# Kernel tuning notes

Measured on AMD Instinct MI355X. Metric: run time of the kernel, lower is better.

The kernel has to match this reference:

```python
import jax, jax.numpy as jnp
import numpy as np


def setup_inputs() -> dict:
    key = jax.random.key(0)
    k1, k2, k3, k4 = jax.random.split(key, 4)
    B, S, D, F = 16, 4096, 1024, 1024
    x = jax.random.normal(k1, (B, S, D), dtype=jnp.float32)
    # Keras 'normal' initializer ~ N(0, 0.05); scale similarly for realism
    W_key = jax.random.normal(k2, (D, F), dtype=jnp.float32) * 0.05
    W_query = jax.random.normal(k3, (D, F), dtype=jnp.float32) * 0.05
    W_value = jax.random.normal(k4, (D, F), dtype=jnp.float32) * 0.05
    return {"x": x, "W_key": W_key, "W_query": W_query, "W_value": W_value}


def reference(x, W_key, W_query, W_value):
    # x: [B,S,D]; W_*: [D,F]
    keys = jnp.tanh(jnp.einsum("bsd,df->bsf", x, W_key))
    query = jnp.tanh(jnp.einsum("bsd,df->bsf", x, W_query))
    value = jnp.tanh(jnp.einsum("bsd,df->bsf", x, W_value))
    # diag(Q K^T) == per-token dot product, computed directly in O(S*F)
    attn_scores = jnp.einsum("bsf,bsf->bs", query, keys)  # [B,S]
    attn_softmax = jax.nn.softmax(attn_scores, axis=-1)[..., None]  # [B,S,1]
    # value^T @ softmax -> [B,F,1]
    weighted_input = jnp.einsum("bsf,bso->bfo", value, attn_softmax)
    return weighted_input, attn_softmax
```

## Files before the change

kernel.cpp:

```cpp
#include <hip/hip_runtime.h>
#include <hip/hip_bf16.h>
#include <math.h>
#include <stdint.h>

typedef _Float16 f16;
typedef _Float16 half8 __attribute__((ext_vector_type(8)));
typedef float f32x4 __attribute__((ext_vector_type(4)));

#define B_ 16
#define S_ 4096
#define D_ 1024
#define F_ 1024
#define TOK (B_*S_)
#define TB3 128
#define FB3 64
#define NFB3 16
#define NT3 32
#define NSV 4
#define CSV (S_/NSV)

__device__ __forceinline__ void gload_lds16(const void* g, void* l) {
    __builtin_amdgcn_global_load_lds(
        (__attribute__((address_space(1))) const unsigned int*)(unsigned long long)(uintptr_t)g,
        (__attribute__((address_space(3))) unsigned int*)(unsigned int)(uintptr_t)l,
        16, 0, 0);
}

__device__ __forceinline__ void fma4(float4& a, float s, const float4& wv) {
    a.x += s * wv.x; a.y += s * wv.y; a.z += s * wv.z; a.w += s * wv.w;
}
__device__ __forceinline__ void wtanh4(float4& acc, float pw, const float4& a) {
    acc.x += pw * tanhf(a.x); acc.y += pw * tanhf(a.y);
    acc.z += pw * tanhf(a.z); acc.w += pw * tanhf(a.w);
}

__global__ void cvt_x(const float* __restrict__ x, f16* __restrict__ xh) {
    size_t i = ((size_t)blockIdx.x * 256 + threadIdx.x) * 8;
    float4 a = *(const float4*)(x + i);
    float4 b = *(const float4*)(x + i + 4);
    half8 h = {(f16)a.x,(f16)a.y,(f16)a.z,(f16)a.w,
               (f16)b.x,(f16)b.y,(f16)b.z,(f16)b.w};
    *(half8*)(xh + i) = h;
}

__global__ void cvt_w2(const float* __restrict__ Wk, const float* __restrict__ Wq,
                       f16* __restrict__ wtf) {
    const int gw   = blockIdx.x * 4 + (threadIdx.x >> 6);
    const int lane = threadIdx.x & 63;
    const int nblk = gw & 3, kt = (gw >> 2) & 31, fb = (gw >> 7) & 15, mat = gw >> 11;
    const float* W = mat ? Wq : Wk;
    const int f  = fb * 64 + nblk * 16 + (lane & 15);
    const int d0 = kt * 32 + (lane >> 4) * 8;
    half8 h;
#pragma unroll
    for (int e = 0; e < 8; ++e) h[e] = (f16)W[(size_t)(d0 + e) * F_ + f];
    *(half8*)(wtf + (size_t)gw * 512 + lane * 8) = h;
}

__launch_bounds__(256, 3)
__global__ void score_gemm(const f16* __restrict__ xh, const f16* __restrict__ wtf,
                           float* __restrict__ part) {
    __shared__ __align__(16) f16 Xs[4][TB3 * 32];
    __shared__ float sred[2][TB3];

    const int hid  = blockIdx.x;
    const int orig = (hid & 7) * 1024 + (hid >> 3);
    const int fb   = orig & 15;
    const int tok0 = (orig >> 4) * TB3;

    const int t = threadIdx.x, lane = t & 63, w = t >> 6;
    const int wr = (w >> 1) * 64;
    const int wc = (w & 1) * 32;

    const int rx0 = t >> 2,         qx0 = (t & 3) ^ ((rx0 >> 1) & 3);
    const int rx1 = (t + 256) >> 2, qx1 = (t & 3) ^ ((rx1 >> 1) & 3);
    const f16* srcX0 = xh + (size_t)(tok0 + rx0) * D_ + qx0 * 8;
    const f16* srcX1 = xh + (size_t)(tok0 + rx1) * D_ + qx1 * 8;
    const int wbase = w * 1024;

    int offA[4];
#pragma unroll
    for (int m = 0; m < 4; ++m) {
        int row = wr + m * 16 + (lane & 15);
        int q   = (lane >> 4) ^ ((row >> 1) & 3);
        offA[m] = row * 32 + q * 8;
    }

    const f16* bK = wtf + (((size_t)fb * NT3 * 4) + 2 * (w & 1)) * 512 + lane * 8;
    const f16* bQ = bK + (size_t)NFB3 * NT3 * 4 * 512;

#define STAGE_X(sl, kof) do {                                         \
        gload_lds16(srcX0 + (kof), (char*)Xs[sl] + wbase);            \
        gload_lds16(srcX1 + (kof), (char*)Xs[sl] + 4096 + wbase);     \
    } while (0)

    f32x4 accK[4][2] = {};
    f32x4 accQ[4][2] = {};
    half8 wKf[2][2], wQf[2][2];

    STAGE_X(0, 0);
    STAGE_X(1, 32);
    STAGE_X(2, 64);
#pragma unroll
    for (int n = 0; n < 2; ++n) {
        wKf[0][n] = *(const half8*)(bK + n * 512);
        wQf[0][n] = *(const half8*)(bQ + n * 512);
    }
    asm volatile("s_waitcnt vmcnt(8)" ::: "memory");
    __builtin_amdgcn_s_barrier();

#pragma unroll
    for (int kt = 0; kt < NT3; ++kt) {
        const int cur = kt & 3, par = kt & 1, nx = par ^ 1;
        if (kt < NT3 - 1) {
#pragma unroll
            for (int n = 0; n < 2; ++n) {
                wKf[nx][n] = *(const half8*)(bK + ((size_t)(kt + 1) * 4 + n) * 512);
                wQf[nx][n] = *(const half8*)(bQ + ((size_t)(kt + 1) * 4 + n) * 512);
            }
        }
        if (kt < NT3 - 3) STAGE_X((kt + 3) & 3, (kt + 3) * 32);

        half8 aF[4];
#pragma unroll
        for (int m = 0; m < 4; ++m) aF[m] = *(const half8*)(Xs[cur] + offA[m]);
#pragma unroll
        for (int n = 0; n < 2; ++n)
#pragma unroll
            for (int m = 0; m < 4; ++m) {
                accK[m][n] = __builtin_amdgcn_mfma_f32_16x16x32_f16(aF[m], wKf[par][n], accK[m][n], 0, 0, 0);
                accQ[m][n] = __builtin_amdgcn_mfma_f32_16x16x32_f16(aF[m], wQf[par][n], accQ[m][n], 0, 0, 0);
            }
        if (kt < NT3 - 1) __builtin_amdgcn_s_barrier();
    }
#undef STAGE_X

#pragma unroll
    for (int m = 0; m < 4; ++m) {
        float s[4] = {0.f, 0.f, 0.f, 0.f};
#pragma unroll
        for (int n = 0; n < 2; ++n)
#pragma unroll
            for (int j = 0; j < 4; ++j)
                s[j] += tanhf(accQ[m][n][j]) * tanhf(accK[m][n][j]);
#pragma unroll
        for (int j = 0; j < 4; ++j) {
            s[j] += __shfl_xor(s[j], 1);
            s[j] += __shfl_xor(s[j], 2);
            s[j] += __shfl_xor(s[j], 4);
            s[j] += __shfl_xor(s[j], 8);
        }
        if ((lane & 15) == 0) {
            int g = lane >> 4;
#pragma unroll
            for (int j = 0; j < 4; ++j)
                sred[w & 1][wr + m * 16 + g * 4 + j] = s[j];
        }
    }
    __syncthreads();
    if (t < TB3)
        part[(size_t)fb * TOK + tok0 + t] = sred[0][t] + sred[1][t];
}

__global__ void sum_k(const float* __restrict__ part, float* __restrict__ scores) {
    int i = blockIdx.x * 256 + threadIdx.x;
    float s = 0.f;
#pragma unroll
    for (int fb = 0; fb < NFB3; ++fb) s += part[(size_t)fb * TOK + i];
    scores[i] = s;
}

__global__ void softmax_k(const float* __restrict__ scores, float* __restrict__ out) {
    __shared__ float sc[S_];
    __shared__ float red[256];
    const int b = blockIdx.x, t = threadIdx.x;
    float lmax = -1e30f;
    for (int i = t; i < S_; i += 256) {
        float s = scores[(size_t)b * S_ + i];
        sc[i] = s;
        lmax = fmaxf(lmax, s);
    }
    red[t] = lmax; __syncthreads();
    for (int o = 128; o > 0; o >>= 1) { if (t < o) red[t] = fmaxf(red[t], red[t + o]); __syncthreads(); }
    const float mx = red[0]; __syncthreads();
    float lsum = 0.f;
    for (int i = t; i < S_; i += 256) { float e = expf(sc[i] - mx); sc[i] = e; lsum += e; }
    red[t] = lsum; __syncthreads();
    for (int o = 128; o > 0; o >>= 1) { if (t < o) red[t] += red[t + o]; __syncthreads(); }
    const float inv = 1.0f / red[0];
    for (int i = t; i < S_; i += 256)
        out[(size_t)B_ * F_ + (size_t)b * S_ + i] = sc[i] * inv;
}

__launch_bounds__(256)
__global__ void value_k4(const float* __restrict__ x, const float* __restrict__ Wv,
                         const float* __restrict__ p_in, float* __restrict__ vpart) {
    __shared__ __align__(16) float xs[8][D_];
    __shared__ float ps[CSV];
    __shared__ int   idxs[CSV];
    __shared__ int   wsum[4];
    __shared__ int   rbase_s;
    const int b = blockIdx.x, c = blockIdx.y;
    const int t = threadIdx.x, lane = t & 63, w = t >> 6;
    const int s0 = c * CSV;

    if (t == 0) rbase_s = 0;
    __syncthreads();
#pragma unroll 1
    for (int r = 0; r < 4; ++r) {
        int i = r * 256 + t;
        float p = p_in[(size_t)b * S_ + s0 + i];
        bool flag = p > 1e-7f;
        unsigned long long mask = __ballot(flag);
        if (lane == 0) wsum[w] = __popcll(mask);
        __syncthreads();
        int base = rbase_s;
#pragma unroll
        for (int k = 0; k < 4; ++k) if (k < w) base += wsum[k];
        if (flag) {
            int pos = base + __popcll(mask & ((1ull << lane) - 1ull));
            idxs[pos] = s0 + i;
            ps[pos] = p;
        }
        __syncthreads();
        if (t == 0) rbase_s += wsum[0] + wsum[1] + wsum[2] + wsum[3];
        __syncthreads();
    }
    const int cnt = rbase_s;

    float4 acc = {0.f, 0.f, 0.f, 0.f};
    for (int g = 0; g < cnt; g += 8) {
        __syncthreads();
#pragma unroll
        for (int r = 0; r < 8; ++r) {
            float4 v = {0.f, 0.f, 0.f, 0.f};
            if (g + r < cnt)
                v = ((const float4*)(x + ((size_t)b * S_ + idxs[g + r]) * D_))[t];
            ((float4*)xs[r])[t] = v;
        }
        __syncthreads();
        float4 a[8] = {};
#pragma unroll 2
        for (int dq = 0; dq < D_ / 4; ++dq) {
            const float* wrp = Wv + (size_t)dq * 4 * F_;
            float4 wv0 = ((const float4*)(wrp        ))[t];
            float4 wv1 = ((const float4*)(wrp + F_   ))[t];
            float4 wv2 = ((const float4*)(wrp + 2*F_ ))[t];
            float4 wv3 = ((const float4*)(wrp + 3*F_ ))[t];
#pragma unroll
            for (int r = 0; r < 8; ++r) {
                float4 xr = ((const float4*)xs[r])[dq];
                fma4(a[r], xr.x, wv0); fma4(a[r], xr.y, wv1);
                fma4(a[r], xr.z, wv2); fma4(a[r], xr.w, wv3);
            }
        }
#pragma unroll
        for (int r = 0; r < 8; ++r)
            if (g + r < cnt) wtanh4(acc, ps[g + r], a[r]);
    }
    ((float4*)(vpart + ((size_t)c * B_ + b) * F_))[t] = acc;
}

__global__ void value_red(const float* __restrict__ vpart, float* __restrict__ out) {
    int i = blockIdx.x * 256 + threadIdx.x;
    float s = 0.f;
#pragma unroll
    for (int c = 0; c < NSV; ++c) s += vpart[(size_t)c * B_ * F_ + i];
    out[i] = s;
}

extern "C" void kernel_launch(void* const* d_in, const int* in_sizes, int n_in,
                              void* d_out, int out_size, void* d_ws, size_t ws_size,
                              hipStream_t stream) {
    const float* x  = (const float*)d_in[0];
    const float* Wk = (const float*)d_in[1];
    const float* Wq = (const float*)d_in[2];
    const float* Wv = (const float*)d_in[3];
    float* out = (float*)d_out;
    char* ws = (char*)d_ws;

    f16*   xh     = (f16*)ws;
    f16*   wtf    = (f16*)(ws + (size_t)TOK * D_ * 2);
    float* part   = (float*)(ws + (size_t)TOK * D_ * 2 + 2 * (size_t)D_ * F_ * 2);
    float* scores = part + (size_t)NFB3 * TOK;

    cvt_x<<<TOK * D_ / 8 / 256, 256, 0, stream>>>(x, xh);
    cvt_w2<<<1024, 256, 0, stream>>>(Wk, Wq, wtf);
    score_gemm<<<NFB3 * (TOK / TB3), 256, 0, stream>>>(xh, wtf, part);
    sum_k<<<TOK / 256, 256, 0, stream>>>(part, scores);
    softmax_k<<<B_, 256, 0, stream>>>(scores, out);
    float* vpart = part;
    const float* p_in = out + (size_t)B_ * F_;
    value_k4<<<dim3(B_, NSV), 256, 0, stream>>>(x, Wv, p_in, vpart);
    value_red<<<B_ * F_ / 256, 256, 0, stream>>>(vpart, out);
}
```

Measured before the change: 575.7 us.

## Retile score GEMM to per-wave private X tiles without block barriers

Changes the score GEMM tile from 128 tokens x 64 features to 256 tokens x 32 features. Each wave now stages its own 64-row X slice into a private triple-buffered LDS region, so the per-k-step block barriers and the cross-wave shared reduction go away, and each wave writes its partial scores directly. It also adds s_setprio around the MFMA burst and per-iteration vmcnt waits. The cost is that each X tile is reused by fewer features, so X is reloaded twice as often per feature, and the partial-score buffer plus the sum_k pass over it double in size.

```diff
diff --git a/kernel.cpp b/kernel.cpp
--- a/kernel.cpp
+++ b/kernel.cpp
@@ -12,9 +12,9 @@
 #define D_ 1024
 #define F_ 1024
 #define TOK (B_*S_)
-#define TB3 128
-#define FB3 64
-#define NFB3 16
+#define TB4 256
+#define FB4 32
+#define NFB4 32
 #define NT3 32
 #define NSV 4
 #define CSV (S_/NSV)
@@ -47,9 +47,9 @@
                        f16* __restrict__ wtf) {
     const int gw   = blockIdx.x * 4 + (threadIdx.x >> 6);
     const int lane = threadIdx.x & 63;
-    const int nblk = gw & 3, kt = (gw >> 2) & 31, fb = (gw >> 7) & 15, mat = gw >> 11;
+    const int n = gw & 1, kt = (gw >> 1) & 31, fb = (gw >> 6) & 31, mat = gw >> 11;
     const float* W = mat ? Wq : Wk;
-    const int f  = fb * 64 + nblk * 16 + (lane & 15);
+    const int f  = fb * 32 + n * 16 + (lane & 15);
     const int d0 = kt * 32 + (lane >> 4) * 8;
     half8 h;
 #pragma unroll
@@ -60,70 +60,77 @@
 __launch_bounds__(256, 3)
 __global__ void score_gemm(const f16* __restrict__ xh, const f16* __restrict__ wtf,
                            float* __restrict__ part) {
-    __shared__ __align__(16) f16 Xs[4][TB3 * 32];
-    __shared__ float sred[2][TB3];
+    __shared__ __align__(16) f16 Xs[4][3][64 * 32];
 
     const int hid  = blockIdx.x;
     const int orig = (hid & 7) * 1024 + (hid >> 3);
-    const int fb   = orig & 15;
-    const int tok0 = (orig >> 4) * TB3;
+    const int fb   = orig & 31;
+    const int tok0 = (orig >> 5) * TB4;
 
     const int t = threadIdx.x, lane = t & 63, w = t >> 6;
-    const int wr = (w >> 1) * 64;
-    const int wc = (w & 1) * 32;
-
-    const int rx0 = t >> 2,         qx0 = (t & 3) ^ ((rx0 >> 1) & 3);
-    const int rx1 = (t + 256) >> 2, qx1 = (t & 3) ^ ((rx1 >> 1) & 3);
-    const f16* srcX0 = xh + (size_t)(tok0 + rx0) * D_ + qx0 * 8;
-    const f16* srcX1 = xh + (size_t)(tok0 + rx1) * D_ + qx1 * 8;
-    const int wbase = w * 1024;
+    const int wr = w * 64;
+
+    const f16* srcX[4];
+#pragma unroll
+    for (int i = 0; i < 4; ++i) {
+        int row = i * 16 + (lane >> 2);
+        int q   = (lane & 3) ^ ((row >> 1) & 3);
+        srcX[i] = xh + (size_t)(tok0 + wr + row) * D_ + q * 8;
+    }
+    f16* ldsbase = &Xs[w][0][0];
 
     int offA[4];
 #pragma unroll
     for (int m = 0; m < 4; ++m) {
-        int row = wr + m * 16 + (lane & 15);
+        int row = m * 16 + (lane & 15);
         int q   = (lane >> 4) ^ ((row >> 1) & 3);
         offA[m] = row * 32 + q * 8;
     }
 
-    const f16* bK = wtf + (((size_t)fb * NT3 * 4) + 2 * (w & 1)) * 512 + lane * 8;
-    const f16* bQ = bK + (size_t)NFB3 * NT3 * 4 * 512;
-
-#define STAGE_X(sl, kof) do {                                         \
-        gload_lds16(srcX0 + (kof), (char*)Xs[sl] + wbase);            \
-        gload_lds16(srcX1 + (kof), (char*)Xs[sl] + 4096 + wbase);     \
+    const f16* bK = wtf + ((size_t)fb * 32) * 2 * 512 + lane * 8;
+    const f16* bQ = bK + (size_t)2048 * 512;
+
+#define STAGE_X(sl, kof) do {                                             \
+        char* xb = (char*)(ldsbase + (sl) * 2048);                        \
+        _Pragma("unroll")                                                 \
+        for (int i_ = 0; i_ < 4; ++i_)                                    \
+            gload_lds16(srcX[i_] + (kof), xb + i_ * 1024);                \
     } while (0)
 
     f32x4 accK[4][2] = {};
     f32x4 accQ[4][2] = {};
     half8 wKf[2][2], wQf[2][2];
 
-    STAGE_X(0, 0);
-    STAGE_X(1, 32);
-    STAGE_X(2, 64);
 #pragma unroll
     for (int n = 0; n < 2; ++n) {
         wKf[0][n] = *(const half8*)(bK + n * 512);
         wQf[0][n] = *(const half8*)(bQ + n * 512);
     }
-    asm volatile("s_waitcnt vmcnt(8)" ::: "memory");
-    __builtin_amdgcn_s_barrier();
+    STAGE_X(0, 0);
+    STAGE_X(1, 32);
 
 #pragma unroll
     for (int kt = 0; kt < NT3; ++kt) {
-        const int cur = kt & 3, par = kt & 1, nx = par ^ 1;
+        const int cur = kt % 3, par = kt & 1, nx = par ^ 1;
+
         if (kt < NT3 - 1) {
 #pragma unroll
             for (int n = 0; n < 2; ++n) {
-                wKf[nx][n] = *(const half8*)(bK + ((size_t)(kt + 1) * 4 + n) * 512);
-                wQf[nx][n] = *(const half8*)(bQ + ((size_t)(kt + 1) * 4 + n) * 512);
+                wKf[nx][n] = *(const half8*)(bK + ((size_t)(kt + 1) * 2 + n) * 512);
+                wQf[nx][n] = *(const half8*)(bQ + ((size_t)(kt + 1) * 2 + n) * 512);
             }
         }
-        if (kt < NT3 - 3) STAGE_X((kt + 3) & 3, (kt + 3) * 32);
+
+        if (kt == 0)            asm volatile("s_waitcnt vmcnt(8)"  ::: "memory");
+        else if (kt == NT3 - 1) asm volatile("s_waitcnt vmcnt(4)"  ::: "memory");
+        else                    asm volatile("s_waitcnt vmcnt(12)" ::: "memory");
 
         half8 aF[4];
 #pragma unroll
-        for (int m = 0; m < 4; ++m) aF[m] = *(const half8*)(Xs[cur] + offA[m]);
+        for (int m = 0; m < 4; ++m)
+            aF[m] = *(const half8*)(ldsbase + cur * 2048 + offA[m]);
+
+        __builtin_amdgcn_s_setprio(1);
 #pragma unroll
         for (int n = 0; n < 2; ++n)
 #pragma unroll
@@ -131,7 +138,9 @@
                 accK[m][n] = __builtin_amdgcn_mfma_f32_16x16x32_f16(aF[m], wKf[par][n], accK[m][n], 0, 0, 0);
                 accQ[m][n] = __builtin_amdgcn_mfma_f32_16x16x32_f16(aF[m], wQf[par][n], accQ[m][n], 0, 0, 0);
             }
-        if (kt < NT3 - 1) __builtin_amdgcn_s_barrier();
+        __builtin_amdgcn_s_setprio(0);
+
+        if (kt < NT3 - 2) STAGE_X((kt + 2) % 3, (kt + 2) * 32);
     }
 #undef STAGE_X
 
@@ -154,19 +163,16 @@
             int g = lane >> 4;
 #pragma unroll
             for (int j = 0; j < 4; ++j)
-                sred[w & 1][wr + m * 16 + g * 4 + j] = s[j];
-        }
-    }
-    __syncthreads();
-    if (t < TB3)
-        part[(size_t)fb * TOK + tok0 + t] = sred[0][t] + sred[1][t];
+                part[(size_t)fb * TOK + tok0 + wr + m * 16 + g * 4 + j] = s[j];
+        }
+    }
 }
 
 __global__ void sum_k(const float* __restrict__ part, float* __restrict__ scores) {
     int i = blockIdx.x * 256 + threadIdx.x;
     float s = 0.f;
 #pragma unroll
-    for (int fb = 0; fb < NFB3; ++fb) s += part[(size_t)fb * TOK + i];
+    for (int fb = 0; fb < NFB4; ++fb) s += part[(size_t)fb * TOK + i];
     scores[i] = s;
 }
 
@@ -282,11 +288,11 @@
     f16*   xh     = (f16*)ws;
     f16*   wtf    = (f16*)(ws + (size_t)TOK * D_ * 2);
     float* part   = (float*)(ws + (size_t)TOK * D_ * 2 + 2 * (size_t)D_ * F_ * 2);
-    float* scores = part + (size_t)NFB3 * TOK;
+    float* scores = part + (size_t)NFB4 * TOK;
 
     cvt_x<<<TOK * D_ / 8 / 256, 256, 0, stream>>>(x, xh);
     cvt_w2<<<1024, 256, 0, stream>>>(Wk, Wq, wtf);
-    score_gemm<<<NFB3 * (TOK / TB3), 256, 0, stream>>>(xh, wtf, part);
+    score_gemm<<<NFB4 * (TOK / TB4), 256, 0, stream>>>(xh, wtf, part);
     sum_k<<<TOK / 256, 256, 0, stream>>>(part, scores);
     softmax_k<<<B_, 256, 0, stream>>>(scores, out);
     float* vpart = part;
```

Result: slower. 685.4 us (+19.1%).
